# Performance work log

Hardware: AMD Instinct MI355X
Metric: run time of the kernel (lower is better)

## Reference

```python
import jax, jax.numpy as jnp
import numpy as np

HEADS = 16
DIM_HEAD = 64
INNER = HEADS * DIM_HEAD  # 1024
QDIM = 1024
CDIM = 1024


def setup_inputs() -> dict:
    key = jax.random.key(0)
    ks = jax.random.split(key, 7)
    x = jax.random.normal(ks[0], (4, 2048, QDIM), dtype=jnp.float32)
    context = jax.random.normal(ks[1], (4, CDIM), dtype=jnp.float32)
    s = 0.02
    Wq = jax.random.normal(ks[2], (QDIM, INNER), dtype=jnp.float32) * s
    Wk = jax.random.normal(ks[3], (CDIM, INNER), dtype=jnp.float32) * s
    Wv = jax.random.normal(ks[4], (CDIM, INNER), dtype=jnp.float32) * s
    Wo = jax.random.normal(ks[5], (INNER, QDIM), dtype=jnp.float32) * s
    bo = jnp.zeros((QDIM,), dtype=jnp.float32)
    return {"x": x, "context": context, "Wq": Wq, "Wk": Wk, "Wv": Wv, "Wo": Wo, "bo": bo}


def reference(x, context, Wq, Wk, Wv, Wo, bo):
    B, N, _ = x.shape
    H, D = HEADS, DIM_HEAD
    scale = D ** (-0.5)
    # implicit cross attention: context (B, C) -> (B, 1, C)
    ctx = context[:, None, :]
    q = (x @ Wq).reshape(B, N, H, D).transpose(0, 2, 1, 3)      # (B,H,N,D)
    k = (ctx @ Wk).reshape(B, 1, H, D).transpose(0, 2, 1, 3)    # (B,H,1,D)
    v = (ctx @ Wv).reshape(B, 1, H, D).transpose(0, 2, 1, 3)
    # implicit cross-attn: prepend context token's k/v, append q as k/v
    k = jnp.concatenate([k, q], axis=2)  # (B,H,N+1,D)
    v = jnp.concatenate([v, q], axis=2)
    M = N + 1
    sim = jnp.einsum('bhid,bhjd->bhij', q, k) * scale  # (B,H,N,M)
    # causal mask with diagonal offset = k_len - q_len (implicit path)
    causal = jnp.tril(jnp.ones((N, M), dtype=bool), k=M - N)
    neg = -jnp.finfo(sim.dtype).max
    sim = jnp.where(causal[None, None], sim, neg)
    attn = jax.nn.softmax(sim, axis=-1)
    out = jnp.einsum('bhij,bhjd->bhid', attn, v)  # (B,H,N,D)
    out = out.transpose(0, 2, 1, 3).reshape(B, N, H * D)
    return out @ Wo + bo
```

## Files before the change

### kernel.cpp

```cpp
#include <hip/hip_runtime.h>
#include <stdint.h>

#define B_ 4
#define N_ 2048
#define H_ 16
#define D_ 64
#define QD 1024
#define SCALE 0.125f
#define LOG2E 1.44269504f
#define SC2 (SCALE * LOG2E)

typedef __bf16 bf16x8 __attribute__((ext_vector_type(8)));
typedef float f32x4 __attribute__((ext_vector_type(4)));
typedef float f32x16 __attribute__((ext_vector_type(16)));
typedef unsigned short u16x8 __attribute__((ext_vector_type(8)));
typedef unsigned short ushort_t;

__device__ __forceinline__ unsigned short f2bf(float f) {
  union { float f; unsigned u; } x; x.f = f;
  unsigned r = (x.u + 0x7fffu + ((x.u >> 16) & 1u)) >> 16;
  return (unsigned short)r;
}

__device__ __forceinline__ void ldg2lds16(const void* g, void* l) {
  __builtin_amdgcn_global_load_lds(
      (const __attribute__((address_space(1))) void*)g,
      (__attribute__((address_space(3))) void*)l, 16, 0, 0);
}

__device__ __forceinline__ ushort_t bfbits(float f) {
  union { __bf16 b; ushort_t u; } x; x.b = (__bf16)f; return x.u;
}

__global__ __launch_bounds__(256) void k_cvt_bf16(const float* __restrict__ in,
                                                  ushort_t* __restrict__ out, int n8) {
  int i = blockIdx.x * 256 + threadIdx.x;
  if (i >= n8) return;
  const float4* p = (const float4*)in + (size_t)i * 2;
  float4 a = p[0], b = p[1];
  u16x8 r;
  r[0] = f2bf(a.x); r[1] = f2bf(a.y); r[2] = f2bf(a.z); r[3] = f2bf(a.w);
  r[4] = f2bf(b.x); r[5] = f2bf(b.y); r[6] = f2bf(b.z); r[7] = f2bf(b.w);
  *((u16x8*)out + i) = r;
}

__global__ __launch_bounds__(256) void k_transpose_w(const float* __restrict__ Wq,
    const float* __restrict__ Wo, ushort_t* __restrict__ WqT, ushort_t* __restrict__ WoT) {
  const float* W = blockIdx.z ? Wo : Wq;
  ushort_t* WT = blockIdx.z ? WoT : WqT;
  __shared__ float tile[64][65];
  int n0 = blockIdx.x * 64, k0 = blockIdx.y * 64;
  int tx = threadIdx.x & 63, ty = threadIdx.x >> 6;
#pragma unroll
  for (int i = 0; i < 64; i += 4)
    tile[ty + i][tx] = W[(size_t)(k0 + ty + i) * QD + n0 + tx];
  __syncthreads();
#pragma unroll
  for (int i = 0; i < 64; i += 4)
    WT[(size_t)(n0 + ty + i) * QD + k0 + tx] = f2bf(tile[tx][ty + i]);
}

__global__ __launch_bounds__(256) void k_transpose_q(const ushort_t* __restrict__ qb,
                                                     ushort_t* __restrict__ qT) {
  const int bh = blockIdx.y, b = bh >> 4, h = bh & 15;
  const int n0 = blockIdx.x * 64;
  const int t = threadIdx.x;
  __shared__ ushort_t tile[64][72];
  const ushort_t* src = qb + ((size_t)b * N_ + n0) * QD + h * D_;
#pragma unroll
  for (int p = 0; p < 2; p++) {
    int r = (t >> 3) + p * 32;
    u16x8 v = *(const u16x8*)&src[(size_t)r * QD + (t & 7) * 8];
    *(u16x8*)&tile[r][(t & 7) * 8] = v;
  }
  __syncthreads();
  ushort_t* dst = qT + (size_t)bh * D_ * N_ + n0;
#pragma unroll
  for (int p = 0; p < 2; p++) {
    int d = (t >> 3) + p * 32;
    union { ushort_t s[8]; u16x8 v; } o;
#pragma unroll
    for (int e = 0; e < 8; e++) o.s[e] = tile[(t & 7) * 8 + e][d];
    *(u16x8*)&dst[(size_t)d * N_ + (t & 7) * 8] = o.v;
  }
}

__global__ __launch_bounds__(256) void k_ctx_partial(const float* __restrict__ ctx,
    const float* __restrict__ Wk, const float* __restrict__ Wv, float* __restrict__ part) {
  int ich = blockIdx.x;
  int ks = blockIdx.y;
  int kv = blockIdx.z;
  const float* W = kv ? Wv : Wk;
  __shared__ float cs[B_][128];
  int t = threadIdx.x;
  for (int i = t; i < B_ * 128; i += 256)
    cs[i >> 7][i & 127] = ctx[(size_t)(i >> 7) * QD + ks * 128 + (i & 127)];
  __syncthreads();
  int col = ich * 256 + t;
  float a0 = 0, a1 = 0, a2 = 0, a3 = 0;
  for (int k = 0; k < 128; k++) {
    float w = W[(size_t)(ks * 128 + k) * QD + col];
    a0 += cs[0][k] * w; a1 += cs[1][k] * w; a2 += cs[2][k] * w; a3 += cs[3][k] * w;
  }
  float* p = part + (size_t)(ks * 2 + kv) * (B_ * QD);
  p[0 * QD + col] = a0; p[1 * QD + col] = a1; p[2 * QD + col] = a2; p[3 * QD + col] = a3;
}

__global__ __launch_bounds__(256) void k_ctx_reduce(const float* __restrict__ part,
    float* __restrict__ kctx, float* __restrict__ vctx) {
  int idx = blockIdx.x * 256 + threadIdx.x;
  int kv = idx >> 12;
  int rest = idx & 4095;
  float acc = 0;
  for (int ks = 0; ks < 8; ks++) acc += part[(size_t)(ks * 2 + kv) * 4096 + rest];
  (kv ? vctx : kctx)[rest] = acc;
}

template <int BF16OUT>
__global__ __launch_bounds__(256) void k_gemm(const ushort_t* __restrict__ A,
    const ushort_t* __restrict__ Bm, ushort_t* __restrict__ Cb, float* __restrict__ Cf,
    const float* __restrict__ bias) {
  __shared__ ushort_t As[128 * 32];
  __shared__ ushort_t Bs[128 * 32];
  const int t = threadIdx.x;
  const int w = t >> 6, l = t & 63;
  const int wr = w >> 1, wc = w & 1;
  const int lr = l & 15, lg = l >> 4;
  const int m0 = blockIdx.y * 128, n0 = blockIdx.x * 128;
  f32x4 acc[4][4] = {};
  for (int k0 = 0; k0 < QD; k0 += 32) {
    ldg2lds16(&A[(size_t)(m0 + (t >> 2)) * QD + k0 + (t & 3) * 8], &As[t * 8]);
    ldg2lds16(&A[(size_t)(m0 + ((t + 256) >> 2)) * QD + k0 + (t & 3) * 8], &As[(t + 256) * 8]);
    ldg2lds16(&Bm[(size_t)(n0 + (t >> 2)) * QD + k0 + (t & 3) * 8], &Bs[t * 8]);
    ldg2lds16(&Bm[(size_t)(n0 + ((t + 256) >> 2)) * QD + k0 + (t & 3) * 8], &Bs[(t + 256) * 8]);
    __syncthreads();
    bf16x8 af[4], bfr[4];
#pragma unroll
    for (int m = 0; m < 4; m++)
      af[m] = *(const bf16x8*)&As[(wr * 64 + m * 16 + lr) * 32 + lg * 8];
#pragma unroll
    for (int n = 0; n < 4; n++)
      bfr[n] = *(const bf16x8*)&Bs[(wc * 64 + n * 16 + lr) * 32 + lg * 8];
#pragma unroll
    for (int m = 0; m < 4; m++)
#pragma unroll
      for (int n = 0; n < 4; n++)
        acc[m][n] = __builtin_amdgcn_mfma_f32_16x16x32_bf16(af[m], bfr[n], acc[m][n], 0, 0, 0);
    __syncthreads();
  }
#pragma unroll
  for (int m = 0; m < 4; m++) {
    int row = m0 + wr * 64 + m * 16 + lg * 4;
#pragma unroll
    for (int n = 0; n < 4; n++) {
      int col = n0 + wc * 64 + n * 16 + lr;
#pragma unroll
      for (int j = 0; j < 4; j++) {
        float v = acc[m][n][j];
        if constexpr (BF16OUT) {
          Cb[(size_t)(row + j) * QD + col] = f2bf(v);
        } else {
          Cf[(size_t)(row + j) * QD + col] = v + bias[col];
        }
      }
    }
  }
}

__global__ __launch_bounds__(256, 2) void k_attn10(
    const ushort_t* __restrict__ q, const ushort_t* __restrict__ qT,
    const float* __restrict__ kctx, const float* __restrict__ vctx,
    ushort_t* __restrict__ att) {
  const int wg = blockIdx.x;
  const int s = wg >> 6;
  const int bh = ((wg & 7) << 3) | ((wg >> 3) & 7);
  const int b = bh >> 4, h = bh & 15;
  const int t = threadIdx.x, w = t >> 6, l = t & 63;
  const int lq = l & 31, hi = l >> 5;

  __shared__ __align__(128) ushort_t Ks[2][2][4096];
  __shared__ __align__(128) ushort_t Vs[2][2][4096];

  const ushort_t* qbase = q + (size_t)b * N_ * QD + h * D_;
  const ushort_t* qtb = qT + (size_t)bh * D_ * N_;
  const float* kc = kctx + bh * D_;
  const float* vc = vctx + bh * D_;

  const int srow = t >> 3;
  const int scol = 8 * ((t & 7) ^ ((t >> 3) & 7));

#pragma unroll 1
  for (int pass = 0; pass < 2; ++pass) {
    const int qt = pass ? 15 - s : s;
    const int i0 = qt * 128;
    const int wq0 = i0 + w * 32;
    const int NI = qt + 1;

    __builtin_amdgcn_s_barrier();

    const ushort_t* stK = qbase + (size_t)srow * QD + scol;
    const ushort_t* stV = qtb + (size_t)srow * N_ + scol;

    auto stage = [&](int pr, int j) {
      ldg2lds16(stK, &Ks[pr][j][t * 8]);
      ldg2lds16(stK + (size_t)32 * QD, &Ks[pr][j][(t + 256) * 8]);
      ldg2lds16(stV, &Vs[pr][j][t * 8]);
      ldg2lds16(stV + (size_t)32 * N_, &Vs[pr][j][(t + 256) * 8]);
      stK += (size_t)64 * QD;
      stV += 64;
    };

    stage(0, 0);
    stage(0, 1);

    bf16x8 qf[4];
#pragma unroll
    for (int kk = 0; kk < 4; kk++)
      qf[kk] = *(const bf16x8*)&qbase[(size_t)(wq0 + lq) * QD + kk * 16 + hi * 8];

    float m2, lsum;
    f32x16 oacc[2];
    {
      float dot = 0.f;
#pragma unroll
      for (int kk = 0; kk < 4; kk++)
#pragma unroll
        for (int j = 0; j < 8; j++)
          dot += (float)qf[kk][j] * kc[kk * 16 + hi * 8 + j];
      dot += __shfl_xor(dot, 32);
      m2 = dot * SC2;
      lsum = 1.0f;
#pragma unroll
      for (int dt = 0; dt < 2; dt++)
#pragma unroll
        for (int r = 0; r < 16; r++)
          oacc[dt][r] = vc[dt * 32 + (r & 3) + 8 * (r >> 2) + 4 * hi];
    }

    auto body = [&](int tt, const char* ksb, const char* vsb) {
      const int j0 = tt * 64;
      if (j0 > wq0 + 31) return;

      f32x16 p[2];
      __builtin_amdgcn_s_setprio(1);
#pragma unroll
      for (int kb = 0; kb < 2; kb++) {
        f32x16 acc = {};
#pragma unroll
        for (int kk = 0; kk < 4; kk++) {
          bf16x8 kf = *(const bf16x8*)(ksb + (l & 31) * 128 + kb * 4096 +
                                       (((kk * 2 + hi) ^ (l & 7)) << 4));
          acc = __builtin_amdgcn_mfma_f32_32x32x16_bf16(kf, qf[kk], acc, 0, 0, 0);
        }
        p[kb] = acc;
      }
      __builtin_amdgcn_s_setprio(0);

      if (j0 + 63 > wq0) {
        const int qrel = wq0 - j0 + lq;
#pragma unroll
        for (int kb = 0; kb < 2; kb++)
#pragma unroll
          for (int r = 0; r < 16; r++) {
            int key = kb * 32 + (r & 3) + 8 * (r >> 2) + 4 * hi;
            if (key > qrel) p[kb][r] = -1e30f;
          }
      }

#pragma unroll
      for (int kb = 0; kb < 2; kb++)
#pragma unroll
        for (int r = 0; r < 16; r++)
          p[kb][r] = __builtin_exp2f(fmaf(p[kb][r], SC2, -m2));
      float s8[8];
#pragma unroll
      for (int r = 0; r < 8; r++)
        s8[r] = (p[0][r] + p[0][r + 8]) + (p[1][r] + p[1][r + 8]);
      float s4a = s8[0] + s8[4], s4b = s8[1] + s8[5];
      float s4c = s8[2] + s8[6], s4d = s8[3] + s8[7];
      float rs = (s4a + s4b) + (s4c + s4d);
      rs += __shfl_xor(rs, 32);
      lsum += rs;

#pragma unroll
      for (int kb = 0; kb < 2; kb++) {
        unsigned u[8];
#pragma unroll
        for (int i = 0; i < 8; i++) {
          float lo = p[kb][2 * i], hi2 = p[kb][2 * i + 1];
          asm("v_cvt_pk_bf16_f32 %0, %1, %2" : "=v"(u[i]) : "v"(lo), "v"(hi2));
        }
        asm("v_permlane32_swap_b32 %0, %1" : "+v"(u[0]), "+v"(u[2]));
        asm("v_permlane32_swap_b32 %0, %1" : "+v"(u[1]), "+v"(u[3]));
        asm("v_permlane32_swap_b32 %0, %1" : "+v"(u[4]), "+v"(u[6]));
        asm("v_permlane32_swap_b32 %0, %1" : "+v"(u[5]), "+v"(u[7]));
        union { unsigned u4[4]; bf16x8 v; } pf0, pf1;
        pf0.u4[0] = u[0]; pf0.u4[1] = u[1]; pf0.u4[2] = u[2]; pf0.u4[3] = u[3];
        pf1.u4[0] = u[4]; pf1.u4[1] = u[5]; pf1.u4[2] = u[6]; pf1.u4[3] = u[7];
        __builtin_amdgcn_s_setprio(1);
#pragma unroll
        for (int ks = 0; ks < 2; ks++) {
          const bf16x8 pf = ks ? pf1.v : pf0.v;
#pragma unroll
          for (int dt = 0; dt < 2; dt++) {
            bf16x8 vf = *(const bf16x8*)(vsb + (l & 31) * 128 + dt * 4096 +
                                         (((kb * 4 + ks * 2 + hi) ^ (l & 7)) << 4));
            oacc[dt] = __builtin_amdgcn_mfma_f32_32x32x16_bf16(vf, pf, oacc[dt], 0, 0, 0);
          }
        }
        __builtin_amdgcn_s_setprio(0);
      }
    };

    for (int it = 0; it < NI; ++it) {
      const int pr = it & 1;
      if (it + 1 < NI) {
        stage(pr ^ 1, 0);
        stage(pr ^ 1, 1);
        asm volatile("s_waitcnt vmcnt(8)" ::: "memory");
      } else {
        asm volatile("s_waitcnt vmcnt(0)" ::: "memory");
      }
      __builtin_amdgcn_s_barrier();

      body(2 * it,     (const char*)&Ks[pr][0][0], (const char*)&Vs[pr][0][0]);
      body(2 * it + 1, (const char*)&Ks[pr][1][0], (const char*)&Vs[pr][1][0]);
    }

    const float inv = 1.0f / lsum;
    ushort_t* ob = att + (size_t)b * N_ * QD + (size_t)(wq0 + lq) * QD + h * D_;
#pragma unroll
    for (int dt = 0; dt < 2; dt++)
#pragma unroll
      for (int rq = 0; rq < 4; rq++) {
        union { ushort_t s4[4]; unsigned long long v; } o;
#pragma unroll
        for (int e = 0; e < 4; e++) o.s4[e] = bfbits(oacc[dt][rq * 4 + e] * inv);
        *(unsigned long long*)(ob + dt * 32 + 8 * rq + 4 * hi) = o.v;
      }
  }
}

extern "C" void kernel_launch(void* const* d_in, const int* in_sizes, int n_in,
                              void* d_out, int out_size, void* d_ws, size_t ws_size,
                              hipStream_t stream) {
  const float* x = (const float*)d_in[0];
  const float* ctx = (const float*)d_in[1];
  const float* Wq = (const float*)d_in[2];
  const float* Wk = (const float*)d_in[3];
  const float* Wv = (const float*)d_in[4];
  const float* Wo = (const float*)d_in[5];
  const float* bo = (const float*)d_in[6];
  float* out = (float*)d_out;

  char* ws = (char*)d_ws;
  size_t off = 0;
  ushort_t* xb = (ushort_t*)(ws + off);   off += (size_t)8192 * 1024 * 2;
  ushort_t* qb = (ushort_t*)(ws + off);   off += (size_t)8192 * 1024 * 2;
  ushort_t* attb = (ushort_t*)(ws + off); off += (size_t)8192 * 1024 * 2;
  ushort_t* WqT = (ushort_t*)(ws + off);  off += (size_t)1024 * 1024 * 2;
  ushort_t* WoT = (ushort_t*)(ws + off);  off += (size_t)1024 * 1024 * 2;
  float* kctx = (float*)(ws + off);       off += (size_t)4096 * 4;
  float* vctx = (float*)(ws + off);       off += (size_t)4096 * 4;
  float* part = (float*)(ws + off);       off += (size_t)16 * 4096 * 4;
  ushort_t* qT = xb;

  k_cvt_bf16<<<dim3(4096), dim3(256), 0, stream>>>(x, xb, 8192 * 1024 / 8);
  k_transpose_w<<<dim3(16, 16, 2), dim3(256), 0, stream>>>(Wq, Wo, WqT, WoT);
  k_ctx_partial<<<dim3(4, 8, 2), dim3(256), 0, stream>>>(ctx, Wk, Wv, part);
  k_ctx_reduce<<<dim3(32), dim3(256), 0, stream>>>(part, kctx, vctx);
  k_gemm<1><<<dim3(8, 64), dim3(256), 0, stream>>>(xb, WqT, qb, nullptr, nullptr);
  k_transpose_q<<<dim3(32, 64), dim3(256), 0, stream>>>(qb, qT);
  k_attn10<<<dim3(512), dim3(256), 0, stream>>>(qb, qT, kctx, vctx, attb);
  k_gemm<0><<<dim3(8, 64), dim3(256), 0, stream>>>(attb, WoT, nullptr, out, bo);
}
```

Baseline: 158.4 us.

## Rewrite GEMM with 128x256 tiles, triple-buffered swizzled LDS pipeline

Replaces the 128x128, single-buffered, 8-warp-less GEMM with a 512-thread kernel that computes 128x256 tiles using a 3-stage LDS ring buffer, a BK of 64, and XOR-swizzled LDS layout. Global loads for stage k+2 are interleaved with the MFMA quarters of stage k, and s_setprio raises priority around the MFMAs. The aim is to hide global memory latency, cut LDS bank conflicts and barrier stalls, and raise reuse per loaded tile. The cost is much more LDS per block (about 144KB), which limits occupancy, and a grid of only 256 blocks.

```diff
diff --git a/kernel.cpp b/kernel.cpp
--- a/kernel.cpp
+++ b/kernel.cpp
@@ -117,37 +117,101 @@
 }
 
 template <int BF16OUT>
-__global__ __launch_bounds__(256) void k_gemm(const ushort_t* __restrict__ A,
+__global__ __launch_bounds__(512, 2) void k_gemm8(const ushort_t* __restrict__ A,
     const ushort_t* __restrict__ Bm, ushort_t* __restrict__ Cb, float* __restrict__ Cf,
     const float* __restrict__ bias) {
-  __shared__ ushort_t As[128 * 32];
-  __shared__ ushort_t Bs[128 * 32];
+  __shared__ ushort_t As[3][128 * 64];
+  __shared__ ushort_t Bs[3][256 * 64];
   const int t = threadIdx.x;
-  const int w = t >> 6, l = t & 63;
-  const int wr = w >> 1, wc = w & 1;
+  const int l = t & 63;
+  const int wid = t >> 6;
+  const int wr = wid >> 2, wc = wid & 3;
   const int lr = l & 15, lg = l >> 4;
-  const int m0 = blockIdx.y * 128, n0 = blockIdx.x * 128;
+  const int m0 = blockIdx.y * 128, n0 = blockIdx.x * 256;
+
   f32x4 acc[4][4] = {};
-  for (int k0 = 0; k0 < QD; k0 += 32) {
-    ldg2lds16(&A[(size_t)(m0 + (t >> 2)) * QD + k0 + (t & 3) * 8], &As[t * 8]);
-    ldg2lds16(&A[(size_t)(m0 + ((t + 256) >> 2)) * QD + k0 + (t & 3) * 8], &As[(t + 256) * 8]);
-    ldg2lds16(&Bm[(size_t)(n0 + (t >> 2)) * QD + k0 + (t & 3) * 8], &Bs[t * 8]);
-    ldg2lds16(&Bm[(size_t)(n0 + ((t + 256) >> 2)) * QD + k0 + (t & 3) * 8], &Bs[(t + 256) * 8]);
-    __syncthreads();
-    bf16x8 af[4], bfr[4];
-#pragma unroll
-    for (int m = 0; m < 4; m++)
-      af[m] = *(const bf16x8*)&As[(wr * 64 + m * 16 + lr) * 32 + lg * 8];
-#pragma unroll
-    for (int n = 0; n < 4; n++)
-      bfr[n] = *(const bf16x8*)&Bs[(wc * 64 + n * 16 + lr) * 32 + lg * 8];
-#pragma unroll
-    for (int m = 0; m < 4; m++)
-#pragma unroll
-      for (int n = 0; n < 4; n++)
-        acc[m][n] = __builtin_amdgcn_mfma_f32_16x16x32_bf16(af[m], bfr[n], acc[m][n], 0, 0, 0);
-    __syncthreads();
-  }
+
+  const int NKS = QD / 64;
+
+  auto stageA = [&](int buf, int k0) {
+#pragma unroll
+    for (int rep = 0; rep < 2; rep++) {
+      int c = t + rep * 512;
+      int row = c >> 3, c0 = 8 * ((c & 7) ^ (row & 7));
+      ldg2lds16(&A[(size_t)(m0 + row) * QD + k0 + c0], &As[buf][c * 8]);
+    }
+  };
+  auto stageB2 = [&](int buf, int k0, int r0) {
+#pragma unroll
+    for (int rep = 0; rep < 2; rep++) {
+      int c = t + (r0 + rep) * 512;
+      int row = c >> 3, c0 = 8 * ((c & 7) ^ (row & 7));
+      ldg2lds16(&Bm[(size_t)(n0 + row) * QD + k0 + c0], &Bs[buf][c * 8]);
+    }
+  };
+
+  stageA(0, 0);
+  stageB2(0, 0, 0); stageB2(0, 0, 2);
+  stageA(1, 64);
+  stageB2(1, 64, 0); stageB2(1, 64, 2);
+  asm volatile("s_waitcnt vmcnt(6)" ::: "memory");
+  __builtin_amdgcn_s_barrier();
+
+  int buf = 0;
+  for (int ks = 0; ks < NKS; ++ks) {
+    int nb = buf + 2; if (nb >= 3) nb -= 3;
+    const int nk0 = (ks + 2) * 64;
+    const char* ab = (const char*)&As[buf][0];
+    const char* bb = (const char*)&Bs[buf][0];
+
+#pragma unroll
+    for (int q = 0; q < 4; q++) {
+      if (ks + 2 < NKS) {
+        if (q == 0) stageA(nb, nk0);
+        else if (q == 1) stageB2(nb, nk0, 0);
+        else if (q == 2) stageB2(nb, nk0, 2);
+      }
+      const int mq = (q >> 1) * 2, nq = (q & 1) * 2;
+      bf16x8 af[2][2], bfq[2][2];
+#pragma unroll
+      for (int mi = 0; mi < 2; mi++) {
+        int row = wr * 64 + (mq + mi) * 16 + lr;
+#pragma unroll
+        for (int kk = 0; kk < 2; kk++)
+          af[mi][kk] = *(const bf16x8*)(ab + row * 128 +
+                                        (((kk * 4 + lg) ^ (row & 7)) << 4));
+      }
+#pragma unroll
+      for (int ni = 0; ni < 2; ni++) {
+        int row = wc * 64 + (nq + ni) * 16 + lr;
+#pragma unroll
+        for (int kk = 0; kk < 2; kk++)
+          bfq[ni][kk] = *(const bf16x8*)(bb + row * 128 +
+                                         (((kk * 4 + lg) ^ (row & 7)) << 4));
+      }
+      __builtin_amdgcn_s_barrier();
+      __builtin_amdgcn_s_setprio(1);
+#pragma unroll
+      for (int mi = 0; mi < 2; mi++)
+#pragma unroll
+        for (int ni = 0; ni < 2; ni++)
+#pragma unroll
+          for (int kk = 0; kk < 2; kk++)
+            acc[mq + mi][nq + ni] = __builtin_amdgcn_mfma_f32_16x16x32_bf16(
+                af[mi][kk], bfq[ni][kk], acc[mq + mi][nq + ni], 0, 0, 0);
+      __builtin_amdgcn_s_setprio(0);
+      if (q == 3) {
+        if (ks + 2 < NKS) {
+          asm volatile("s_waitcnt vmcnt(6)" ::: "memory");
+        } else if (ks + 1 < NKS) {
+          asm volatile("s_waitcnt vmcnt(0)" ::: "memory");
+        }
+      }
+      __builtin_amdgcn_s_barrier();
+    }
+    buf = (buf == 2) ? 0 : buf + 1;
+  }
+
 #pragma unroll
   for (int m = 0; m < 4; m++) {
     int row = m0 + wr * 64 + m * 16 + lg * 4;
@@ -369,8 +433,8 @@
   k_transpose_w<<<dim3(16, 16, 2), dim3(256), 0, stream>>>(Wq, Wo, WqT, WoT);
   k_ctx_partial<<<dim3(4, 8, 2), dim3(256), 0, stream>>>(ctx, Wk, Wv, part);
   k_ctx_reduce<<<dim3(32), dim3(256), 0, stream>>>(part, kctx, vctx);
-  k_gemm<1><<<dim3(8, 64), dim3(256), 0, stream>>>(xb, WqT, qb, nullptr, nullptr);
+  k_gemm8<1><<<dim3(4, 64), dim3(512), 0, stream>>>(xb, WqT, qb, nullptr, nullptr);
   k_transpose_q<<<dim3(32, 64), dim3(256), 0, stream>>>(qb, qT);
   k_attn10<<<dim3(512), dim3(256), 0, stream>>>(qb, qT, kctx, vctx, attb);
-  k_gemm<0><<<dim3(8, 64), dim3(256), 0, stream>>>(attb, WoT, nullptr, out, bo);
-}
+  k_gemm8<0><<<dim3(4, 64), dim3(512), 0, stream>>>(attb, WoT, nullptr, out, bo);
+}
```

New measurement: 183.5 us. +15.8%, slower.
